# Optimization experiments

Measured on AMD Instinct MI355X. Metric: run time of the kernel, lower is better.

The kernel has to match this reference:

```python
import jax, jax.numpy as jnp
import numpy as np

N_HEAD = 8
D_MODEL = 512


def setup_inputs() -> dict:
    key = jax.random.key(0)
    ks = jax.random.split(key, 9)
    B, S, D, H = 4, 1024, D_MODEL, N_HEAD
    s = 1.0 / np.sqrt(D)
    return {
        "x": jax.random.normal(ks[0], (B, S, D), dtype=jnp.float32),
        "Wq": jax.random.normal(ks[1], (D, H * D), dtype=jnp.float32) * s,
        "bq": jnp.zeros((H * D,), jnp.float32),
        "Wk": jax.random.normal(ks[2], (D, H * D), dtype=jnp.float32) * s,
        "bk": jnp.zeros((H * D,), jnp.float32),
        "Wv": jax.random.normal(ks[3], (D, H * D), dtype=jnp.float32) * s,
        "bv": jnp.zeros((H * D,), jnp.float32),
        "Wo": jax.random.normal(ks[4], (H * D, D), dtype=jnp.float32) * (1.0 / np.sqrt(H * D)),
        "bo": jnp.zeros((D,), jnp.float32),
    }


def reference(x, Wq, bq, Wk, bk, Wv, bv, Wo, bo):
    B, S, D = x.shape
    H = N_HEAD
    # QKV projections, split into heads: [B, S, H, D] (each head uses full d_model)
    q = (x @ Wq + bq).reshape(B, S, H, D)
    k = (x @ Wk + bk).reshape(B, S, H, D)
    v = (x @ Wv + bv).reshape(B, S, H, D)
    # scores: [H, B, Sq, Sk], scaled by 1/d_model (scale=d_model in original)
    scores = jnp.einsum("bqhd,bkhd->hbqk", q, k) / D
    attn = jax.nn.softmax(scores, axis=-1)
    # context: [B, Sq, H, D] -> concat heads -> output projection
    ctx = jnp.einsum("hbqk,bkhd->bqhd", attn, v).reshape(B, S, H * D)
    out = ctx @ Wo + bo
    # attn returned as [(H*B), Sq, Sk] matching torch head-major layout
    return out, attn.reshape(H * B, S, S)
```

## Files before the change

kernel.cpp:

```cpp
#include <hip/hip_runtime.h>
#include <hip/hip_bf16.h>


typedef unsigned short u16;
typedef __attribute__((ext_vector_type(8))) short short8;
typedef __attribute__((ext_vector_type(4))) float f32x4;
typedef __attribute__((ext_vector_type(2))) unsigned int u32x2;

#define BK 32

__device__ __forceinline__ u16 f2bf(float f) {
    union { float f; unsigned u; } v; v.f = f;
    unsigned u = v.u;
    u += 0x7fffu + ((u >> 16) & 1u);
    return (u16)(u >> 16);
}

__device__ __forceinline__ void gl2lds16(const void* g, void* l) {
    __builtin_amdgcn_global_load_lds(
        (const __attribute__((address_space(1))) void*)g,
        (__attribute__((address_space(3))) void*)l, 16, 0, 0);
}

template<int MF, int NF, bool AF32, bool OUTF32, bool ROWBIAS>
__global__ __launch_bounds__(256)
void gemm_bt(const void* __restrict__ Ap, int lda, long long sAh, long long sAb,
             const u16* __restrict__ Bp, int ldb, long long sBh, long long sBb,
             void* __restrict__ Cp, int ldc, long long sCh, long long sCb,
             int K, const float* __restrict__ bias, long long sbias,
             float scale, int nb)
{
    constexpr int BMt = MF * 32, BNt = NF * 32;
    constexpr int AW = AF32 ? 2 * BK : BK;
    __shared__ __attribute__((aligned(16))) u16 Alds[2][BMt][AW];
    __shared__ __attribute__((aligned(16))) u16 Blds[2][BNt][BK];

    const int z  = blockIdx.z;
    const int zh = z / nb, zb = z % nb;

    const int m0 = blockIdx.y * BMt;
    const int n0 = blockIdx.x * BNt;

    const int tid  = threadIdx.x;
    const int lane = tid & 63;
    const int wave = tid >> 6;
    const int wm = (wave >> 1) * (MF * 16);
    const int wn = (wave & 1) * (NF * 16);

    const float* Afp = (const float*)Ap + (long long)zh * sAh + (long long)zb * sAb;
    const u16*   Abf = (const u16*)Ap + (long long)zh * sAh + (long long)zb * sAb;
    const u16*   Bbf = Bp + (long long)zh * sBh + (long long)zb * sBb;

    f32x4 acc[MF][NF] = {};

    auto stage = [&](int buf, int kt) {
        if (AF32) {
            #pragma unroll
            for (int i = 0; i < BMt / 32; ++i) {
                int idx = i * 256 + tid;
                int row = idx >> 3;
                int c   = idx & 7;
                int cs  = c ^ (row & 7);
                gl2lds16(Afp + (long long)(m0 + row) * lda + kt + (cs << 2),
                         (u16*)&Alds[buf][0][0] + idx * 8);
            }
        } else {
            #pragma unroll
            for (int i = 0; i < BMt / 64; ++i) {
                int idx = i * 256 + tid;
                int row = idx >> 2;
                int kq  = (idx & 3) << 3;
                gl2lds16(Abf + (long long)(m0 + row) * lda + (kt + kq),
                         &Alds[buf][row][kq]);
            }
        }
        #pragma unroll
        for (int i = 0; i < BNt / 64; ++i) {
            int idx = i * 256 + tid;
            int row = idx >> 2;
            int kq  = (idx & 3) << 3;
            gl2lds16(Bbf + (long long)(n0 + row) * ldb + (kt + kq),
                     &Blds[buf][row][kq]);
        }
    };

    const int nt = K / BK;
    stage(0, 0);

    for (int t = 0; t < nt; ++t) {
        const int cur = t & 1;
        __syncthreads();
        if (t + 1 < nt)
            stage(cur ^ 1, (t + 1) * BK);

        const int kq = (lane >> 4) << 3;
        const int fr = lane & 15;
        short8 af[MF], bfr[NF];
        if (AF32) {
            const int c0 = (lane >> 4) << 1;
            #pragma unroll
            for (int im = 0; im < MF; ++im) {
                int row = wm + im * 16 + fr;
                int s   = row & 7;
                const float* ar = (const float*)&Alds[cur][row][0];
                f32x4 lo = *(const f32x4*)(ar + (((c0    ) ^ s) << 2));
                f32x4 hi = *(const f32x4*)(ar + (((c0 + 1) ^ s) << 2));
                union { short8 v; __hip_bfloat162 h[4]; } a;
                a.h[0] = __float22bfloat162_rn(make_float2(lo.x, lo.y));
                a.h[1] = __float22bfloat162_rn(make_float2(lo.z, lo.w));
                a.h[2] = __float22bfloat162_rn(make_float2(hi.x, hi.y));
                a.h[3] = __float22bfloat162_rn(make_float2(hi.z, hi.w));
                af[im] = a.v;
            }
        } else {
            #pragma unroll
            for (int im = 0; im < MF; ++im)
                af[im] = *(const short8*)(&Alds[cur][wm + im * 16 + fr][kq]);
        }
        #pragma unroll
        for (int in = 0; in < NF; ++in)
            bfr[in] = *(const short8*)(&Blds[cur][wn + in * 16 + fr][kq]);
        #pragma unroll
        for (int im = 0; im < MF; ++im)
            #pragma unroll
            for (int in = 0; in < NF; ++in)
                acc[im][in] = __builtin_amdgcn_mfma_f32_16x16x32_bf16(
                    af[im], bfr[in], acc[im][in], 0, 0, 0);
    }

    float* Cfp = (float*)Cp + (long long)zh * sCh + (long long)zb * sCb;
    u16*   Cbf = (u16*)Cp + (long long)zh * sCh + (long long)zb * sCb;
    const float* biasp = bias ? bias + (long long)zh * sbias : nullptr;
    const int rb  = (lane >> 4) << 2;
    const int col = lane & 15;
    #pragma unroll
    for (int im = 0; im < MF; ++im) {
        #pragma unroll
        for (int r = 0; r < 4; ++r) {
            int row = m0 + wm + im * 16 + rb + r;
            float rbias = (biasp && ROWBIAS) ? biasp[row] : 0.0f;
            #pragma unroll
            for (int in = 0; in < NF; ++in) {
                int cc = n0 + wn + in * 16 + col;
                float v = acc[im][in][r] * scale;
                if (biasp) v += ROWBIAS ? rbias : biasp[cc];
                if (OUTF32) Cfp[(long long)row * ldc + cc] = v;
                else        Cbf[(long long)row * ldc + cc] = f2bf(v);
            }
        }
    }
}

__global__ __launch_bounds__(256)
void softmax_kernel(float* __restrict__ attn)
{
    const long long row = blockIdx.x;
    float* p = attn + row * 1024;
    const int tid  = threadIdx.x;
    const int lane = tid & 63;
    const int wave = tid >> 6;
    __shared__ float red[8];

    f32x4 v = *(f32x4*)(p + tid * 4);
    float mx = fmaxf(fmaxf(v.x, v.y), fmaxf(v.z, v.w));
    #pragma unroll
    for (int off = 1; off < 64; off <<= 1)
        mx = fmaxf(mx, __shfl_xor(mx, off, 64));
    if (lane == 0) red[wave] = mx;
    __syncthreads();
    mx = fmaxf(fmaxf(red[0], red[1]), fmaxf(red[2], red[3]));

    v.x = __expf(v.x - mx);
    v.y = __expf(v.y - mx);
    v.z = __expf(v.z - mx);
    v.w = __expf(v.w - mx);
    float s = v.x + v.y + v.z + v.w;
    #pragma unroll
    for (int off = 1; off < 64; off <<= 1)
        s += __shfl_xor(s, off, 64);
    if (lane == 0) red[4 + wave] = s;
    __syncthreads();
    s = red[4] + red[5] + red[6] + red[7];
    float inv = 1.0f / s;
    v.x *= inv; v.y *= inv; v.z *= inv; v.w *= inv;
    *(f32x4*)(p + tid * 4) = v;
}

__global__ __launch_bounds__(256)
void cvt_kernel(const float* __restrict__ in, u16* __restrict__ out)
{
    long long i = (long long)blockIdx.x * 256 + threadIdx.x;
    f32x4 v = *(const f32x4*)(in + i * 4);
    u32x2 p;
    p.x = (unsigned)f2bf(v.x) | ((unsigned)f2bf(v.y) << 16);
    p.y = (unsigned)f2bf(v.z) | ((unsigned)f2bf(v.w) << 16);
    *(u32x2*)(out + i * 4) = p;
}

__global__ __launch_bounds__(256)
void wtrans_kernel(const float* __restrict__ in, u16* __restrict__ out, int R, int C)
{
    __shared__ __attribute__((aligned(16))) u16 t[64][72];
    const int r0 = blockIdx.y * 64, c0 = blockIdx.x * 64;
    const int tid = threadIdx.x;
    const int lr = tid >> 4;
    const int lc = (tid & 15) << 2;
    #pragma unroll
    for (int j = 0; j < 4; ++j) {
        int rr = lr + j * 16;
        f32x4 v = *(const f32x4*)(in + (long long)(r0 + rr) * C + c0 + lc);
        u32x2 p;
        p.x = (unsigned)f2bf(v.x) | ((unsigned)f2bf(v.y) << 16);
        p.y = (unsigned)f2bf(v.z) | ((unsigned)f2bf(v.w) << 16);
        *(u32x2*)(&t[rr][lc]) = p;
    }
    __syncthreads();
    const int oc = tid >> 2;
    const int rs = (tid & 3) << 4;
    union { short8 v; u16 e[8]; } a, b;
    #pragma unroll
    for (int j = 0; j < 8; ++j) a.e[j] = t[rs + j][oc];
    #pragma unroll
    for (int j = 0; j < 8; ++j) b.e[j] = t[rs + 8 + j][oc];
    u16* o = out + (long long)(c0 + oc) * R + r0 + rs;
    *(short8*)o = a.v;
    *(short8*)(o + 8) = b.v;
}

extern "C" void kernel_launch(void* const* d_in, const int* in_sizes, int n_in,
                              void* d_out, int out_size, void* d_ws, size_t ws_size,
                              hipStream_t stream)
{
    const float* x  = (const float*)d_in[0];
    const float* Wq = (const float*)d_in[1];
    const float* bq = (const float*)d_in[2];
    const float* Wk = (const float*)d_in[3];
    const float* bk = (const float*)d_in[4];
    const float* Wv = (const float*)d_in[5];
    const float* bv = (const float*)d_in[6];
    const float* Wo = (const float*)d_in[7];
    const float* bo = (const float*)d_in[8];

    const int B = 4, S = 1024, D = 512, H = 8;
    const int HD = H * D;
    const int BS = B * S;

    float* out  = (float*)d_out;
    float* attn = out + (long long)BS * D;

    u16* xb   = (u16*)d_ws;
    u16* WqT  = xb  + (long long)BS * D;
    u16* WkT  = WqT + (long long)HD * D;
    u16* WvT  = WkT + (long long)HD * D;
    u16* WoT  = WvT + (long long)HD * D;
    u16* buf1 = WoT + (long long)D * HD;
    u16* buf2 = buf1 + (long long)BS * HD;

    dim3 blk(256);

    cvt_kernel<<<dim3(BS * D / 1024), blk, 0, stream>>>(x, xb);
    wtrans_kernel<<<dim3(HD / 64, D / 64), blk, 0, stream>>>(Wq, WqT, D, HD);
    wtrans_kernel<<<dim3(HD / 64, D / 64), blk, 0, stream>>>(Wk, WkT, D, HD);
    wtrans_kernel<<<dim3(HD / 64, D / 64), blk, 0, stream>>>(Wv, WvT, D, HD);
    wtrans_kernel<<<dim3(D / 64, HD / 64), blk, 0, stream>>>(Wo, WoT, HD, D);

    {
        dim3 g(HD / 128, BS / 128, 1);
        gemm_bt<4,4,false,false,false><<<g, blk, 0, stream>>>(
            xb, D, 0, 0, WqT, D, 0, 0, buf1, HD, 0, 0, D, bq, 0, 1.0f, 1);
        gemm_bt<4,4,false,false,false><<<g, blk, 0, stream>>>(
            xb, D, 0, 0, WkT, D, 0, 0, buf2, HD, 0, 0, D, bk, 0, 1.0f, 1);
    }
    {
        dim3 g(S / 128, S / 128, H * B);
        gemm_bt<4,4,false,true,false><<<g, blk, 0, stream>>>(
            buf1, HD, D, (long long)S * HD,
            buf2, HD, D, (long long)S * HD,
            attn, S, (long long)B * S * S, (long long)S * S,
            D, nullptr, 0, 1.0f / (float)D, B);
    }
    softmax_kernel<<<dim3(H * B * S), blk, 0, stream>>>(attn);
    {
        dim3 g(S / 128, D / 128, H * B);
        gemm_bt<4,4,false,false,true><<<g, blk, 0, stream>>>(
            WvT, D, (long long)D * D, 0,
            xb, D, 0, (long long)S * D,
            buf1, S, (long long)B * D * S, (long long)D * S,
            D, bv, D, 1.0f, B);
    }
    {
        dim3 g(D / 256, S / 128, H * B);
        gemm_bt<4,8,true,false,false><<<g, blk, 0, stream>>>(
            attn, S, (long long)B * S * S, (long long)S * S,
            buf1, S, (long long)B * D * S, (long long)D * S,
            buf2, HD, D, (long long)S * HD,
            S, nullptr, 0, 1.0f, B);
    }
    {
        dim3 g(D / 128, BS / 64, 1);
        gemm_bt<2,4,false,true,false><<<g, blk, 0, stream>>>(
            buf2, HD, 0, 0, WoT, HD, 0, 0, out, D, 0, 0, HD, bo, 0, 1.0f, 1);
    }
}
```

Baseline: 549.6 us.

## Remap workgroups across XCDs and use single-buffered smaller tiles for PV GEMM

```diff
diff --git a/kernel.cpp b/kernel.cpp
--- a/kernel.cpp
+++ b/kernel.cpp
@@ -22,7 +22,7 @@
         (__attribute__((address_space(3))) void*)l, 16, 0, 0);
 }
 
-template<int MF, int NF, bool AF32, bool OUTF32, bool ROWBIAS>
+template<int MF, int NF, bool AF32, bool OUTF32, bool ROWBIAS, bool DBUF>
 __global__ __launch_bounds__(256)
 void gemm_bt(const void* __restrict__ Ap, int lda, long long sAh, long long sAb,
              const u16* __restrict__ Bp, int ldb, long long sBh, long long sBb,
@@ -32,14 +32,24 @@
 {
     constexpr int BMt = MF * 32, BNt = NF * 32;
     constexpr int AW = AF32 ? 2 * BK : BK;
-    __shared__ __attribute__((aligned(16))) u16 Alds[2][BMt][AW];
-    __shared__ __attribute__((aligned(16))) u16 Blds[2][BNt][BK];
-
-    const int z  = blockIdx.z;
-    const int zh = z / nb, zb = z % nb;
-
-    const int m0 = blockIdx.y * BMt;
-    const int n0 = blockIdx.x * BNt;
+    constexpr int NB = DBUF ? 2 : 1;
+    __shared__ __attribute__((aligned(16))) u16 Alds[NB][BMt][AW];
+    __shared__ __attribute__((aligned(16))) u16 Blds[NB][BNt][BK];
+
+    int bx = blockIdx.x, by = blockIdx.y, bz = blockIdx.z;
+    {
+        const int gx = gridDim.x, gy = gridDim.y;
+        const int nwg = gx * gy * (int)gridDim.z;
+        const int wgid = bx + gx * (by + gy * bz);
+        const int xcd = wgid & 7, lp = wgid >> 3;
+        const int q = nwg >> 3, r = nwg & 7;
+        int nid = (xcd < r ? xcd * (q + 1) : r * (q + 1) + (xcd - r) * q) + lp;
+        bx = nid % gx; nid /= gx; by = nid % gy; bz = nid / gy;
+    }
+
+    const int zh = bz / nb, zb = bz % nb;
+    const int m0 = by * BMt;
+    const int n0 = bx * BNt;
 
     const int tid  = threadIdx.x;
     const int lane = tid & 63;
@@ -84,15 +94,7 @@
         }
     };
 
-    const int nt = K / BK;
-    stage(0, 0);
-
-    for (int t = 0; t < nt; ++t) {
-        const int cur = t & 1;
-        __syncthreads();
-        if (t + 1 < nt)
-            stage(cur ^ 1, (t + 1) * BK);
-
+    auto compute = [&](int buf) {
         const int kq = (lane >> 4) << 3;
         const int fr = lane & 15;
         short8 af[MF], bfr[NF];
@@ -102,7 +104,7 @@
             for (int im = 0; im < MF; ++im) {
                 int row = wm + im * 16 + fr;
                 int s   = row & 7;
-                const float* ar = (const float*)&Alds[cur][row][0];
+                const float* ar = (const float*)&Alds[buf][row][0];
                 f32x4 lo = *(const f32x4*)(ar + (((c0    ) ^ s) << 2));
                 f32x4 hi = *(const f32x4*)(ar + (((c0 + 1) ^ s) << 2));
                 union { short8 v; __hip_bfloat162 h[4]; } a;
@@ -115,17 +117,36 @@
         } else {
             #pragma unroll
             for (int im = 0; im < MF; ++im)
-                af[im] = *(const short8*)(&Alds[cur][wm + im * 16 + fr][kq]);
+                af[im] = *(const short8*)(&Alds[buf][wm + im * 16 + fr][kq]);
         }
         #pragma unroll
         for (int in = 0; in < NF; ++in)
-            bfr[in] = *(const short8*)(&Blds[cur][wn + in * 16 + fr][kq]);
+            bfr[in] = *(const short8*)(&Blds[buf][wn + in * 16 + fr][kq]);
         #pragma unroll
         for (int im = 0; im < MF; ++im)
             #pragma unroll
             for (int in = 0; in < NF; ++in)
                 acc[im][in] = __builtin_amdgcn_mfma_f32_16x16x32_bf16(
                     af[im], bfr[in], acc[im][in], 0, 0, 0);
+    };
+
+    const int nt = K / BK;
+    if (DBUF) {
+        stage(0, 0);
+        for (int t = 0; t < nt; ++t) {
+            const int cur = t & 1;
+            __syncthreads();
+            if (t + 1 < nt)
+                stage(cur ^ 1, (t + 1) * BK);
+            compute(cur);
+        }
+    } else {
+        for (int t = 0; t < nt; ++t) {
+            __syncthreads();
+            stage(0, t * BK);
+            __syncthreads();
+            compute(0);
+        }
     }
 
     float* Cfp = (float*)Cp + (long long)zh * sCh + (long long)zb * sCb;
@@ -266,14 +287,14 @@
 
     {
         dim3 g(HD / 128, BS / 128, 1);
-        gemm_bt<4,4,false,false,false><<<g, blk, 0, stream>>>(
+        gemm_bt<4,4,false,false,false,true><<<g, blk, 0, stream>>>(
             xb, D, 0, 0, WqT, D, 0, 0, buf1, HD, 0, 0, D, bq, 0, 1.0f, 1);
-        gemm_bt<4,4,false,false,false><<<g, blk, 0, stream>>>(
+        gemm_bt<4,4,false,false,false,true><<<g, blk, 0, stream>>>(
             xb, D, 0, 0, WkT, D, 0, 0, buf2, HD, 0, 0, D, bk, 0, 1.0f, 1);
     }
     {
         dim3 g(S / 128, S / 128, H * B);
-        gemm_bt<4,4,false,true,false><<<g, blk, 0, stream>>>(
+        gemm_bt<4,4,false,true,false,true><<<g, blk, 0, stream>>>(
             buf1, HD, D, (long long)S * HD,
             buf2, HD, D, (long long)S * HD,
             attn, S, (long long)B * S * S, (long long)S * S,
@@ -282,15 +303,15 @@
     softmax_kernel<<<dim3(H * B * S), blk, 0, stream>>>(attn);
     {
         dim3 g(S / 128, D / 128, H * B);
-        gemm_bt<4,4,false,false,true><<<g, blk, 0, stream>>>(
+        gemm_bt<4,4,false,false,true,true><<<g, blk, 0, stream>>>(
             WvT, D, (long long)D * D, 0,
             xb, D, 0, (long long)S * D,
             buf1, S, (long long)B * D * S, (long long)D * S,
             D, bv, D, 1.0f, B);
     }
     {
-        dim3 g(D / 256, S / 128, H * B);
-        gemm_bt<4,8,true,false,false><<<g, blk, 0, stream>>>(
+        dim3 g(D / 128, S / 128, H * B);
+        gemm_bt<4,4,true,false,false,false><<<g, blk, 0, stream>>>(
             attn, S, (long long)B * S * S, (long long)S * S,
             buf1, S, (long long)B * D * S, (long long)D * S,
             buf2, HD, D, (long long)S * HD,
@@ -298,7 +319,7 @@
     }
     {
         dim3 g(D / 128, BS / 64, 1);
-        gemm_bt<2,4,false,true,false><<<g, blk, 0, stream>>>(
+        gemm_bt<2,4,false,true,false,true><<<g, blk, 0, stream>>>(
             buf2, HD, 0, 0, WoT, HD, 0, 0, out, D, 0, 0, HD, bo, 0, 1.0f, 1);
     }
 }
```

New measurement: 518.4 us. -5.7%, faster.
